# Optimization experiments

Measured on AMD Instinct MI355X. Metric: run time of the kernel, lower is better.

Reference implementation:

```python
import jax, jax.numpy as jnp
import numpy as np

V, N, D, HEADS = 4, 1536, 256, 4


def setup_inputs() -> dict:
    key = jax.random.key(0)
    ks = jax.random.split(key, 8)
    s = 0.05  # weight init scale
    return {
        "H": jax.random.normal(ks[0], (V, N, D), jnp.float32),
        "C": jax.random.normal(ks[1], (V, V, N, N), jnp.float32),
        "WQ": jax.random.normal(ks[2], (V, D, D), jnp.float32) * s,
        "WK": jax.random.normal(ks[3], (V, D, D), jnp.float32) * s,
        "WV": jax.random.normal(ks[4], (V, D, D), jnp.float32) * s,
        "in_proj_w": jax.random.normal(ks[5], (3 * D, D), jnp.float32) * s,
        "in_proj_b": jnp.zeros((3 * D,), jnp.float32),
        "out_proj_w": jax.random.normal(ks[6], (D, D), jnp.float32) * s,
        "out_proj_b": jnp.zeros((D,), jnp.float32),
        "alphas": jnp.full((V,), 0.95, jnp.float32),
        "alpha_align": jnp.asarray(0.5, jnp.float32),
        "beta": jnp.asarray(0.5, jnp.float32),
        "topk": 32,
    }


def _ircva(H, in_proj_w, in_proj_b, out_proj_w, out_proj_b, alphas):
    # torch MultiheadAttention, seq=V, batch=N, embed=D, heads=HEADS
    dh = D // HEADS
    qkv = jnp.einsum('snd,ed->sne', H, in_proj_w) + in_proj_b  # (V,N,3D)
    q, k, v = jnp.split(qkv, 3, axis=-1)
    q = q.reshape(V, N, HEADS, dh)
    k = k.reshape(V, N, HEADS, dh)
    v = v.reshape(V, N, HEADS, dh)
    att = jnp.einsum('snhd,tnhd->nhst', q, k) / jnp.sqrt(jnp.float32(dh))
    w = jax.nn.softmax(att, axis=-1)
    o = jnp.einsum('nhst,tnhd->snhd', w, v).reshape(V, N, D)
    fusion = jnp.einsum('snd,ed->sne', o, out_proj_w) + out_proj_b
    a = alphas[:, None, None]
    return fusion * a + (1.0 - a) * H  # (V,N,D)


def _crcva(aligned, C, WQ, WK, WV, K):
    # per-view projections: Linear y = x @ W.T
    Qn = jnp.einsum('vnd,ved->vne', aligned, WQ)
    Kn = jnp.einsum('vnd,ved->vne', aligned, WK)
    Vn = jnp.einsum('vnd,ved->vne', aligned, WV)
    # per-row top-k sparsification of C[p,q]
    vals, idx = jax.lax.top_k(C, K)  # (V,V,N,K)
    Cf = C.reshape(-1, N)
    rows = jnp.arange(Cf.shape[0])[:, None]
    sparse = jnp.zeros_like(Cf).at[rows, idx.reshape(-1, K)].set(vals.reshape(-1, K))
    sparse = sparse.reshape(V, V, N, N)
    row_sum = sparse.sum(axis=-1, keepdims=True) + 1e-12
    C_hat = sparse / row_sum
    # diagonal (p==q) pairs are left as zeros in the torch code
    offdiag = (1.0 - jnp.eye(V, dtype=C.dtype))[:, :, None, None]
    C_hat = C_hat * offdiag
    mask = (C_hat > 0).astype(C.dtype)
    scores = jnp.einsum('pnd,qmd->pqnm', Qn, Kn) / jnp.sqrt(jnp.float32(D))
    scores = scores * mask + (1.0 - mask) * (-1e9)
    alpha_nbr = jax.nn.softmax(scores, axis=-1)
    return jnp.einsum('pqnm,qmd->pnd', alpha_nbr, Vn)  # (V,N,D)


def reference(H, C, WQ, WK, WV, in_proj_w, in_proj_b, out_proj_w, out_proj_b,
              alphas, alpha_align, beta, topk):
    aligned = _ircva(H, in_proj_w, in_proj_b, out_proj_w, out_proj_b, alphas)
    nbr = _crcva(aligned, C, WQ, WK, WV, int(topk))
    a = jax.nn.sigmoid(alpha_align)
    f_fuse = jax.nn.relu(a * aligned + (1.0 - a) * nbr)
    return beta * H + (1.0 - beta) * f_fuse  # (V,N,D)
```

## Files before the change

### kernel.cpp

```cpp
#include <hip/hip_runtime.h>
#include <hip/hip_bf16.h>
#include <math.h>

typedef __bf16 bf16x8 __attribute__((ext_vector_type(8)));
typedef __bf16 bf16x4 __attribute__((ext_vector_type(4)));
typedef float  f32x4  __attribute__((ext_vector_type(4)));

static constexpr int kV = 4;
static constexpr int kN = 1536;
static constexpr int kD = 256;
static constexpr int kTopK = 32;

__global__ __launch_bounds__(256) void convert_kernel(
    const float* __restrict__ H, const float* __restrict__ inW,
    const float* __restrict__ outW, const float* __restrict__ WQ,
    const float* __restrict__ WK, const float* __restrict__ WV,
    __bf16* __restrict__ Hb, __bf16* __restrict__ inWb,
    __bf16* __restrict__ outWb, __bf16* __restrict__ Wqkvb,
    float* __restrict__ Vmean)
{
    if (blockIdx.x == 0) {
        f32x4 z = {0.f, 0.f, 0.f, 0.f};
        *(f32x4*)(Vmean + threadIdx.x * 4) = z;
    }
    int idx = (blockIdx.x * 256 + threadIdx.x) * 4;
    const float* src; __bf16* dst; int off;
    if      (idx < 1572864) { src = H;    dst = Hb;             off = idx; }
    else if (idx < 1769472) { src = inW;  dst = inWb;           off = idx - 1572864; }
    else if (idx < 1835008) { src = outW; dst = outWb;          off = idx - 1769472; }
    else if (idx < 2097152) { src = WQ;   dst = Wqkvb;          off = idx - 1835008; }
    else if (idx < 2359296) { src = WK;   dst = Wqkvb + 262144; off = idx - 2097152; }
    else                    { src = WV;   dst = Wqkvb + 524288; off = idx - 2359296; }
    f32x4 v = *(const f32x4*)(src + off);
    bf16x4 b;
#pragma unroll
    for (int j = 0; j < 4; ++j) b[j] = (__bf16)v[j];
    *(bf16x4*)(dst + off) = b;
}

__global__ __launch_bounds__(256) void gemm_qkv_kernel(
    const __bf16* __restrict__ A, const __bf16* __restrict__ Bm,
    const float* __restrict__ bias, __bf16* __restrict__ outB)
{
    const int Nc = 768, K = 256;
    int wave = blockIdx.x * 4 + (threadIdx.x >> 6);
    int tm  = wave / 12;
    int tn4 = wave - tm * 12;
    int lane = threadIdx.x & 63;
    int r    = lane & 15;
    int quad = lane >> 4;
    const __bf16* Ap = A + (size_t)(tm * 32 + r) * K + quad * 8;
    const __bf16* Bp = Bm + (size_t)(tn4 * 64 + r) * K + quad * 8;
    f32x4 acc[2][4] = {};
    for (int k0 = 0; k0 < K; k0 += 32) {
        bf16x8 a0 = *(const bf16x8*)(Ap + k0);
        bf16x8 a1 = *(const bf16x8*)(Ap + (size_t)16 * K + k0);
#pragma unroll
        for (int t = 0; t < 4; ++t) {
            bf16x8 b = *(const bf16x8*)(Bp + (size_t)t * 16 * K + k0);
            acc[0][t] = __builtin_amdgcn_mfma_f32_16x16x32_bf16(a0, b, acc[0][t], 0, 0, 0);
            acc[1][t] = __builtin_amdgcn_mfma_f32_16x16x32_bf16(a1, b, acc[1][t], 0, 0, 0);
        }
    }
#pragma unroll
    for (int t = 0; t < 4; ++t) {
        int gn = tn4 * 64 + t * 16 + r;
        float bv = bias[gn];
#pragma unroll
        for (int mt = 0; mt < 2; ++mt)
#pragma unroll
            for (int i = 0; i < 4; ++i) {
                int gm = tm * 32 + mt * 16 + quad * 4 + i;
                outB[(size_t)gm * Nc + gn] = (__bf16)(acc[mt][t][i] + bv);
            }
    }
}

__global__ __launch_bounds__(256) void attg3_kernel(
    const __bf16* __restrict__ qkv, const __bf16* __restrict__ outWb,
    const float* __restrict__ outBias, const float* __restrict__ H,
    const float* __restrict__ alphas,
    float* __restrict__ alignedF, __bf16* __restrict__ alignedB)
{
    __shared__ __bf16 obuf[16][280];
    int n0 = blockIdx.x * 4;
    int tid = threadIdx.x;
    int h = tid >> 6, d = tid & 63;
#pragma unroll
    for (int ni = 0; ni < 4; ++ni) {
        int n = n0 + ni;
        float q[4], k[4], vv[4];
#pragma unroll
        for (int s = 0; s < 4; ++s) {
            size_t base = (size_t)(s * kN + n) * 768 + h * 64 + d;
            q[s]  = (float)qkv[base];
            k[s]  = (float)qkv[base + 256];
            vv[s] = (float)qkv[base + 512];
        }
        float att[4][4];
#pragma unroll
        for (int s = 0; s < 4; ++s)
#pragma unroll
            for (int t = 0; t < 4; ++t) {
                float p = q[s] * k[t];
#pragma unroll
                for (int off = 32; off > 0; off >>= 1) p += __shfl_xor(p, off);
                att[s][t] = p * 0.125f;
            }
#pragma unroll
        for (int s = 0; s < 4; ++s) {
            float mx = fmaxf(fmaxf(att[s][0], att[s][1]), fmaxf(att[s][2], att[s][3]));
            float e0 = __expf(att[s][0] - mx), e1 = __expf(att[s][1] - mx);
            float e2 = __expf(att[s][2] - mx), e3 = __expf(att[s][3] - mx);
            float inv = 1.f / (e0 + e1 + e2 + e3);
            float ov = (e0 * vv[0] + e1 * vv[1] + e2 * vv[2] + e3 * vv[3]) * inv;
            obuf[s * 4 + ni][h * 64 + d] = (__bf16)ov;
        }
    }
    __syncthreads();
    int w = tid >> 6, lane = tid & 63;
    int r = lane & 15, quad = lane >> 4;
    f32x4 acc[4] = {};
    for (int k0 = 0; k0 < 256; k0 += 32) {
        bf16x8 a = *(const bf16x8*)&obuf[r][quad * 8 + k0];
#pragma unroll
        for (int t = 0; t < 4; ++t) {
            bf16x8 b = *(const bf16x8*)(outWb + (size_t)(w * 64 + t * 16 + r) * 256 + quad * 8 + k0);
            acc[t] = __builtin_amdgcn_mfma_f32_16x16x32_bf16(a, b, acc[t], 0, 0, 0);
        }
    }
#pragma unroll
    for (int t = 0; t < 4; ++t) {
        int gn = w * 64 + t * 16 + r;
        float bv = outBias[gn];
#pragma unroll
        for (int i = 0; i < 4; ++i) {
            int rl = quad * 4 + i;
            int s = rl >> 2, ni = rl & 3;
            size_t gr = (size_t)(s * kN + n0 + ni);
            float a_ = alphas[s];
            size_t off = gr * kD + gn;
            float res = a_ * (acc[t][i] + bv) + (1.f - a_) * H[off];
            alignedF[off] = res;
            alignedB[off] = (__bf16)res;
        }
    }
}

__global__ __launch_bounds__(256) void gemm_qkv3_kernel(
    const __bf16* __restrict__ A, const __bf16* __restrict__ W,
    __bf16* __restrict__ O0, __bf16* __restrict__ O1, __bf16* __restrict__ O2,
    float* __restrict__ Vmean)
{
    int proj = blockIdx.y;
    __bf16* Ob = (proj == 0) ? O0 : (proj == 1) ? O1 : O2;
    const __bf16* Wb = W + (size_t)proj * 4 * 65536;
    int b = blockIdx.x;
    int view = b / 48;
    int tn4 = threadIdx.x >> 6;
    int lane = threadIdx.x & 63;
    int r = lane & 15, quad = lane >> 4;
    const __bf16* Ap = A + (size_t)(b * 32 + r) * kD + quad * 8;
    const __bf16* Bp = Wb + (size_t)view * 65536 + (size_t)(tn4 * 64 + r) * kD + quad * 8;
    f32x4 acc[2][4] = {};
    for (int k0 = 0; k0 < kD; k0 += 32) {
        bf16x8 a0 = *(const bf16x8*)(Ap + k0);
        bf16x8 a1 = *(const bf16x8*)(Ap + (size_t)16 * kD + k0);
#pragma unroll
        for (int t = 0; t < 4; ++t) {
            bf16x8 bb = *(const bf16x8*)(Bp + (size_t)t * 16 * kD + k0);
            acc[0][t] = __builtin_amdgcn_mfma_f32_16x16x32_bf16(a0, bb, acc[0][t], 0, 0, 0);
            acc[1][t] = __builtin_amdgcn_mfma_f32_16x16x32_bf16(a1, bb, acc[1][t], 0, 0, 0);
        }
    }
#pragma unroll
    for (int t = 0; t < 4; ++t) {
        int gn = tn4 * 64 + t * 16 + r;
#pragma unroll
        for (int mt = 0; mt < 2; ++mt)
#pragma unroll
            for (int i = 0; i < 4; ++i) {
                int gm = b * 32 + mt * 16 + quad * 4 + i;
                Ob[(size_t)gm * kD + gn] = (__bf16)acc[mt][t][i];
            }
    }
    if (proj == 2) {
#pragma unroll
        for (int t = 0; t < 4; ++t) {
            float cs = 0.f;
#pragma unroll
            for (int mt = 0; mt < 2; ++mt)
#pragma unroll
                for (int i = 0; i < 4; ++i) cs += acc[mt][t][i];
            cs += __shfl_xor(cs, 16);
            cs += __shfl_xor(cs, 32);
            if (quad == 0)
                atomicAdd(&Vmean[view * kD + tn4 * 64 + t * 16 + r], cs * (1.f / 1536.f));
        }
    }
}

__global__ __launch_bounds__(256) void crcva_kernel(
    const float* __restrict__ C,
    const __bf16* __restrict__ Qn, const __bf16* __restrict__ Kn,
    const __bf16* __restrict__ Vn, const float* __restrict__ Vmean,
    const float* __restrict__ alignedF, const float* __restrict__ H,
    const float* __restrict__ alpha_align, const float* __restrict__ beta,
    float* __restrict__ out)
{
    int n = blockIdx.x, p = blockIdx.y, tid = threadIdx.x;
    int w = tid >> 6, lane = tid & 63;
    __shared__ unsigned int hist[3][256];
    __shared__ unsigned int idxl[3][kTopK];
    __shared__ unsigned int scnt[3];
    __shared__ float qsh[kD];
    __shared__ float wsh[96];
    __shared__ int   osh[96];
    __shared__ float part[4][kD];

    if (w < 3) {
        int q = w + (w >= p ? 1 : 0);
        const float* row = C + ((size_t)((p * kV + q) * kN + n)) * kN;
        unsigned int key[24];
#pragma unroll
        for (int j = 0; j < 24; ++j) {
            unsigned int u = __float_as_uint(row[j * 64 + lane]);
            key[j] = (u & 0x80000000u) ? ~u : (u | 0x80000000u);
        }
        if (lane == 0) scnt[w] = 0;
        unsigned int pref = 0, need = kTopK;
#pragma unroll
        for (int pass = 0; pass < 4; ++pass) {
            const int shift = 24 - 8 * pass;
#pragma unroll
            for (int k2 = 0; k2 < 4; ++k2) hist[w][lane + k2 * 64] = 0;
            __builtin_amdgcn_wave_barrier();
#pragma unroll
            for (int j = 0; j < 24; ++j) {
                unsigned int k = key[j];
                bool match = (pass == 0) || (((k ^ pref) >> (shift + 8)) == 0);
                if (match) atomicAdd(&hist[w][(k >> shift) & 255u], 1u);
            }
            __builtin_amdgcn_wave_barrier();
            unsigned int h0 = hist[w][lane*4+0], h1 = hist[w][lane*4+1];
            unsigned int h2 = hist[w][lane*4+2], h3 = hist[w][lane*4+3];
            unsigned int s3 = h3, s2 = h2 + s3, s1 = h1 + s2, s0 = h0 + s1;
            unsigned int run = s0;
#pragma unroll
            for (int off = 1; off < 64; off <<= 1) {
                unsigned int v = __shfl_down(run, off);
                if (lane + off < 64) run += v;
            }
            unsigned int above = run - s0;
            unsigned int suf[4]  = {above+s0, above+s1, above+s2, above+s3};
            unsigned int sufN[4] = {above+s1, above+s2, above+s3, above};
            unsigned int pk = 0;
#pragma unroll
            for (int k2 = 0; k2 < 4; ++k2)
                if (suf[k2] >= need && sufN[k2] < need)
                    pk = ((unsigned int)(lane*4 + k2) << 16) | sufN[k2];
#pragma unroll
            for (int off = 1; off < 64; off <<= 1) pk |= __shfl_xor(pk, off);
            pref |= (pk >> 16) << shift;
            need -= (pk & 0xffffu);
        }
        unsigned int T = pref;
        unsigned int eqBefore = 0;
#pragma unroll
        for (int j = 0; j < 24; ++j) {
            unsigned int k = key[j];
            bool e = (k == T);
            unsigned long long m = __ballot(e);
            unsigned int rank = eqBefore + (unsigned int)__popcll(m & ((1ull << lane) - 1ull));
            bool take = (k > T) || (e && rank < need);
            if (take && k > 0x80000000u) {
                unsigned int pos = atomicAdd(&scnt[w], 1u);
                idxl[w][pos] = (unsigned int)(j * 64 + lane);
            }
            eqBefore += (unsigned int)__popcll(m);
        }
    } else {
        bf16x4 qv = *(const bf16x4*)(Qn + ((size_t)p * kN + n) * kD + lane * 4);
#pragma unroll
        for (int e = 0; e < 4; ++e) qsh[lane * 4 + e] = (float)qv[e];
    }
    __syncthreads();

    if (tid < 192) {
        int j = tid >> 1, half = tid & 1;
        int g = j >> 5, r = j & 31;
        int q = g + (g >= p ? 1 : 0);
        int cnt = (int)scnt[g];
        bool valid = (r < cnt);
        int m = valid ? (int)idxl[g][r] : 0;
        int off = valid ? (q * kN + m) * kD : 0;
        float s = 0.f;
        if (valid) {
            const __bf16* kr = Kn + off + half * 128;
            const float*  qh = qsh + half * 128;
            float a0 = 0.f, a1 = 0.f, a2 = 0.f, a3 = 0.f;
#pragma unroll
            for (int dd = 0; dd < 128; dd += 32) {
                bf16x8 k0 = *(const bf16x8*)(kr + dd);
                bf16x8 k1 = *(const bf16x8*)(kr + dd + 8);
                bf16x8 k2 = *(const bf16x8*)(kr + dd + 16);
                bf16x8 k3 = *(const bf16x8*)(kr + dd + 24);
                const float* q0 = qh + dd;
#pragma unroll
                for (int e = 0; e < 8; ++e) {
                    a0 += q0[e]      * (float)k0[e];
                    a1 += q0[e + 8]  * (float)k1[e];
                    a2 += q0[e + 16] * (float)k2[e];
                    a3 += q0[e + 24] * (float)k3[e];
                }
            }
            s = (a0 + a1) + (a2 + a3);
        }
        s += __shfl_xor(s, 1);
        float sc = valid ? s * 0.0625f : -1e30f;
        float mx = sc;
#pragma unroll
        for (int o2 = 2; o2 <= 32; o2 <<= 1) mx = fmaxf(mx, __shfl_xor(mx, o2));
        float e = valid ? __expf(sc - mx) : 0.f;
        float ss = e;
#pragma unroll
        for (int o2 = 2; o2 <= 32; o2 <<= 1) ss += __shfl_xor(ss, o2);
        if (half == 0) {
            wsh[j] = (ss > 0.f) ? e / ss : 0.f;
            osh[j] = off;
        }
    }
    __syncthreads();

    {
        int half32 = lane >> 5, l32 = lane & 31;
        float a[8] = {};
#pragma unroll
        for (int it = 0; it < 12; ++it) {
            int j = w * 24 + it * 2 + half32;
            float wt = wsh[j];
            bf16x8 v = *(const bf16x8*)(Vn + osh[j] + l32 * 8);
#pragma unroll
            for (int e = 0; e < 8; ++e) a[e] += wt * (float)v[e];
        }
#pragma unroll
        for (int e = 0; e < 8; ++e) a[e] += __shfl_xor(a[e], 32);
        if (half32 == 0) {
#pragma unroll
            for (int e = 0; e < 8; ++e) part[w][l32 * 8 + e] = a[e];
        }
    }
    __syncthreads();

    float acc = Vmean[p * kD + tid]
              + part[0][tid] + part[1][tid] + part[2][tid] + part[3][tid];
    float aa = 1.f / (1.f + __expf(-alpha_align[0]));
    float bt = beta[0];
    size_t off = ((size_t)p * kN + n) * kD + tid;
    float al = alignedF[off];
    float f  = fmaxf(aa * al + (1.f - aa) * acc, 0.f);
    out[off] = H[off] * bt + (1.f - bt) * f;
}

extern "C" void kernel_launch(void* const* d_in, const int* in_sizes, int n_in,
                              void* d_out, int out_size, void* d_ws, size_t ws_size,
                              hipStream_t stream)
{
    const float* H        = (const float*)d_in[0];
    const float* C        = (const float*)d_in[1];
    const float* WQ       = (const float*)d_in[2];
    const float* WK       = (const float*)d_in[3];
    const float* WV       = (const float*)d_in[4];
    const float* inW      = (const float*)d_in[5];
    const float* inB      = (const float*)d_in[6];
    const float* outW     = (const float*)d_in[7];
    const float* outBias  = (const float*)d_in[8];
    const float* alphas   = (const float*)d_in[9];
    const float* alpha_al = (const float*)d_in[10];
    const float* beta     = (const float*)d_in[11];
    float* out = (float*)d_out;

    char* w = (char*)d_ws;
    __bf16* Hb       = (__bf16*)w;  w += (size_t)6144 * 256 * 2;
    __bf16* inWb     = (__bf16*)w;  w += (size_t)768 * 256 * 2;
    __bf16* outWb    = (__bf16*)w;  w += (size_t)256 * 256 * 2;
    __bf16* Wqkvb    = (__bf16*)w;  w += (size_t)3 * 4 * 256 * 256 * 2;
    __bf16* qkv      = (__bf16*)w;  w += (size_t)6144 * 768 * 2;
    __bf16* alignedB = (__bf16*)w;  w += (size_t)6144 * 256 * 2;
    float*  alignedF = (float*)w;   w += (size_t)6144 * 256 * 4;
    __bf16* Qn       = (__bf16*)w;  w += (size_t)6144 * 256 * 2;
    __bf16* Kn       = (__bf16*)w;  w += (size_t)6144 * 256 * 2;
    __bf16* Vn       = (__bf16*)w;  w += (size_t)6144 * 256 * 2;
    float*  Vmean    = (float*)w;   w += (size_t)4 * 256 * 4;

    convert_kernel<<<2560, 256, 0, stream>>>(H, inW, outW, WQ, WK, WV,
                                             Hb, inWb, outWb, Wqkvb, Vmean);
    gemm_qkv_kernel<<<576, 256, 0, stream>>>(Hb, inWb, inB, qkv);
    attg3_kernel<<<384, 256, 0, stream>>>(qkv, outWb, outBias, H, alphas,
                                          alignedF, alignedB);
    gemm_qkv3_kernel<<<dim3(192, 3), 256, 0, stream>>>(alignedB, Wqkvb,
                                                       Qn, Kn, Vn, Vmean);
    crcva_kernel<<<dim3(1536, 4), 256, 0, stream>>>(C, Qn, Kn, Vn, Vmean,
        alignedF, H, alpha_al, beta, out);
}
```

Before: 377.7 us.

## Vectorize C row loads, remap grid, and streamline radix top-k selection

The crcva kernel now reads each C row with 16-byte nontemporal vector loads and flattens the grid to 1D, interleaving views and adjacent rows across consecutive blocks. The radix select filters non-positive keys in the first pass and clamps need. It publishes the chosen bin through shared memory instead of a six-step shuffle reduction, and pads the histogram. When the tie count equals the remaining need, a fast path skips the ballot-based ranking. These target the dominant C streaming traffic and the per-row selection overhead, at the cost of more complex control flow and a changed element ordering of indices.

```diff
diff --git a/kernel.cpp b/kernel.cpp
--- a/kernel.cpp
+++ b/kernel.cpp
@@ -208,9 +208,14 @@
     const float* __restrict__ alpha_align, const float* __restrict__ beta,
     float* __restrict__ out)
 {
-    int n = blockIdx.x, p = blockIdx.y, tid = threadIdx.x;
+    int gid = blockIdx.x;
+    int j8  = gid & 7;
+    int p   = j8 & 3;
+    int n   = ((gid >> 3) << 1) | (j8 >> 2);
+    int tid = threadIdx.x;
     int w = tid >> 6, lane = tid & 63;
-    __shared__ unsigned int hist[3][256];
+    __shared__ unsigned int hist[3][257];
+    __shared__ unsigned int sbin[3];
     __shared__ unsigned int idxl[3][kTopK];
     __shared__ unsigned int scnt[3];
     __shared__ float qsh[kD];
@@ -223,9 +228,13 @@
         const float* row = C + ((size_t)((p * kV + q) * kN + n)) * kN;
         unsigned int key[24];
 #pragma unroll
-        for (int j = 0; j < 24; ++j) {
-            unsigned int u = __float_as_uint(row[j * 64 + lane]);
-            key[j] = (u & 0x80000000u) ? ~u : (u | 0x80000000u);
+        for (int j = 0; j < 6; ++j) {
+            f32x4 v4 = __builtin_nontemporal_load((const f32x4*)(row + j * 256 + lane * 4));
+#pragma unroll
+            for (int e = 0; e < 4; ++e) {
+                unsigned int u = __float_as_uint(v4[e]);
+                key[j * 4 + e] = (u & 0x80000000u) ? ~u : (u | 0x80000000u);
+            }
         }
         if (lane == 0) scnt[w] = 0;
         unsigned int pref = 0, need = kTopK;
@@ -233,12 +242,14 @@
         for (int pass = 0; pass < 4; ++pass) {
             const int shift = 24 - 8 * pass;
 #pragma unroll
-            for (int k2 = 0; k2 < 4; ++k2) hist[w][lane + k2 * 64] = 0;
+            for (int k2 = 0; k2 < 4; ++k2) hist[w][lane * 4 + k2] = 0;
+            if (lane == 0) sbin[w] = 0;
             __builtin_amdgcn_wave_barrier();
 #pragma unroll
             for (int j = 0; j < 24; ++j) {
                 unsigned int k = key[j];
-                bool match = (pass == 0) || (((k ^ pref) >> (shift + 8)) == 0);
+                bool match = (pass == 0) ? (k > 0x80000000u)
+                                         : (((k ^ pref) >> (shift + 8)) == 0);
                 if (match) atomicAdd(&hist[w][(k >> shift) & 255u], 1u);
             }
             __builtin_amdgcn_wave_barrier();
@@ -251,33 +262,62 @@
                 unsigned int v = __shfl_down(run, off);
                 if (lane + off < 64) run += v;
             }
+            if (pass == 0) {
+                unsigned int tot = __shfl(run, 0);
+                need = need < tot ? need : tot;
+            }
             unsigned int above = run - s0;
             unsigned int suf[4]  = {above+s0, above+s1, above+s2, above+s3};
             unsigned int sufN[4] = {above+s1, above+s2, above+s3, above};
-            unsigned int pk = 0;
 #pragma unroll
             for (int k2 = 0; k2 < 4; ++k2)
                 if (suf[k2] >= need && sufN[k2] < need)
-                    pk = ((unsigned int)(lane*4 + k2) << 16) | sufN[k2];
-#pragma unroll
-            for (int off = 1; off < 64; off <<= 1) pk |= __shfl_xor(pk, off);
+                    sbin[w] = ((unsigned int)(lane*4 + k2) << 16) | sufN[k2];
+            __builtin_amdgcn_wave_barrier();
+            unsigned int pk = sbin[w];
             pref |= (pk >> 16) << shift;
             need -= (pk & 0xffffu);
+            __builtin_amdgcn_wave_barrier();
         }
         unsigned int T = pref;
-        unsigned int eqBefore = 0;
-#pragma unroll
-        for (int j = 0; j < 24; ++j) {
-            unsigned int k = key[j];
-            bool e = (k == T);
-            unsigned long long m = __ballot(e);
-            unsigned int rank = eqBefore + (unsigned int)__popcll(m & ((1ull << lane) - 1ull));
-            bool take = (k > T) || (e && rank < need);
-            if (take && k > 0x80000000u) {
-                unsigned int pos = atomicAdd(&scnt[w], 1u);
-                idxl[w][pos] = (unsigned int)(j * 64 + lane);
-            }
-            eqBefore += (unsigned int)__popcll(m);
+        unsigned int eq = 0;
+#pragma unroll
+        for (int j = 0; j < 24; ++j) eq += (key[j] == T) ? 1u : 0u;
+#pragma unroll
+        for (int off = 1; off < 64; off <<= 1) eq += __shfl_xor(eq, off);
+        if (eq == need) {
+#pragma unroll
+            for (int j = 0; j < 24; ++j) {
+                unsigned int k = key[j];
+                if (k >= T && k > 0x80000000u) {
+                    unsigned int pos = atomicAdd(&scnt[w], 1u);
+                    idxl[w][pos] = (unsigned int)((j >> 2) * 256 + lane * 4 + (j & 3));
+                }
+            }
+        } else {
+            unsigned int eqBefore = 0;
+            unsigned long long below = (1ull << lane) - 1ull;
+            for (int j4 = 0; j4 < 6; ++j4) {
+                unsigned long long m[4];
+#pragma unroll
+                for (int e = 0; e < 4; ++e) m[e] = __ballot(key[j4 * 4 + e] == T);
+#pragma unroll
+                for (int e = 0; e < 4; ++e) {
+                    unsigned int k = key[j4 * 4 + e];
+                    unsigned int rank = eqBefore;
+#pragma unroll
+                    for (int e2 = 0; e2 < 4; ++e2) rank += (unsigned int)__popcll(m[e2] & below);
+                    for (int e2 = 0; e2 < e; ++e2) rank += (unsigned int)((m[e2] >> lane) & 1ull);
+                    bool iseq = (k == T);
+                    bool take = (k > T) || (iseq && rank < need);
+                    if (take && k > 0x80000000u) {
+                        unsigned int pos = atomicAdd(&scnt[w], 1u);
+                        idxl[w][pos] = (unsigned int)(j4 * 256 + lane * 4 + e);
+                    }
+                }
+                eqBefore += (unsigned int)(__popcll(m[0]) + __popcll(m[1])
+                                         + __popcll(m[2]) + __popcll(m[3]));
+            }
         }
     } else {
         bf16x4 qv = *(const bf16x4*)(Qn + ((size_t)p * kN + n) * kD + lane * 4);
@@ -400,6 +440,6 @@
                                           alignedF, alignedB);
     gemm_qkv3_kernel<<<dim3(192, 3), 256, 0, stream>>>(alignedB, Wqkvb,
                                                        Qn, Kn, Vn, Vmean);
-    crcva_kernel<<<dim3(1536, 4), 256, 0, stream>>>(C, Qn, Kn, Vn, Vmean,
+    crcva_kernel<<<6144, 256, 0, stream>>>(C, Qn, Kn, Vn, Vmean,
         alignedF, H, alpha_al, beta, out);
 }
```

After: 368.9 us. -2.3%, faster.
